# Kernel tuning notes

Measured on AMD Instinct MI355X. Metric: run time of the kernel, lower is better.

The kernel has to match this reference:

```python
import jax, jax.numpy as jnp
import numpy as np

N_OBJS = 15
C_OUT = 2
KP_THRES = 0.95
IOU_THRES = 0.45
N_R, N_SHP, N_EXP = 9, 199, 29
PDIM = N_R + N_SHP + N_EXP
RESIZE = 320
NUM_ANCHORS = 2
SENTINEL = -1e30  # marks non-detected candidate boxes so they never match NMS output


def _anchor_centers(stride):
    hw = RESIZE // stride
    X, Y = jnp.meshgrid(jnp.arange(hw), jnp.arange(hw))
    ac = (jnp.stack([X, Y], -1) * stride).reshape(-1, 2)
    # stack([c]*2, axis=1).reshape(-1,2) == interleaved repeat
    return jnp.repeat(ac, NUM_ANCHORS, axis=0).astype(jnp.float32)  # (A,2)


def _process_level(cls, bbox, param, stride, pms, u_base, shp_base, exp_base, r):
    B, A, _ = cls.shape
    prob = jax.nn.sigmoid(cls)                      # (B,A,2)
    mask = prob > KP_THRES
    ac = _anchor_centers(stride)                    # (A,2)
    d = bbox * stride
    x1 = ac[:, 0] - d[..., 0]; y1 = ac[:, 1] - d[..., 1]
    x2 = ac[:, 0] + d[..., 2]; y2 = ac[:, 1] + d[..., 3]
    boxes = jnp.stack([x1, y1, x2, y2], -1).reshape(B, A, 2, 2)   # rows [x1,y1],[x2,y2]
    # 3DMM param decode
    p = param * pms[1] + pms[0]
    R = p[..., :N_R].reshape(B, A, 3, 3)
    shp = p[..., N_R:N_R + N_SHP]
    exp = p[..., N_R + N_SHP:]
    ln = u_base[:, 0] + shp @ shp_base.T + exp @ exp_base.T       # (B,A,204)
    ln = jnp.einsum('bakd,bacd->bakc', ln.reshape(B, A, 68, 3), R)[..., :2]  # lnmks @ R^T, keep xy
    tl = ln.min(-2, keepdims=True); br = ln.max(-2, keepdims=True)
    scale = (boxes[:, :, 1:, :] - boxes[:, :, :1, :]) / (br - tl)
    ln = jnp.abs(scale) * ln                         # (B,A,68,2)
    boxes_yx = boxes[..., ::-1] * r                  # (x,y)->(y,x), scale to original image
    ln_yx = ln[..., ::-1] * r
    boxes5 = jnp.concatenate(
        [jnp.broadcast_to(boxes_yx.reshape(B, A, 1, 4), (B, A, C_OUT, 4)), prob[..., None]], -1)
    ln_c = jnp.broadcast_to(ln_yx[:, :, None], (B, A, C_OUT, 68, 2))
    bidx = jnp.broadcast_to(jnp.arange(B)[:, None, None], (B, A, C_OUT)).reshape(-1)
    cidx = jnp.broadcast_to(jnp.arange(C_OUT)[None, None, :], (B, A, C_OUT)).reshape(-1)
    return mask.reshape(-1), boxes5.reshape(-1, 5), ln_c.reshape(-1, 68, 2), bidx, cidx


def _greedy_nms(boxes, scores, k, iou_thres):
    # NMS selection indices are constants w.r.t. AD (like tf.image NMS)
    boxes = jax.lax.stop_gradient(boxes)
    scores = jax.lax.stop_gradient(scores)
    n = scores.shape[0]
    area = jnp.clip(boxes[:, 2] - boxes[:, 0], 0) * jnp.clip(boxes[:, 3] - boxes[:, 1], 0)

    def step(carry, i):
        active, sel = carry
        s = jnp.where(active, scores, -jnp.inf)
        j = jnp.argmax(s)
        valid = s[j] > -jnp.inf
        sel = sel.at[i].set(jnp.where(valid, j.astype(jnp.int32), -1))
        tl = jnp.maximum(boxes[j, :2], boxes[:, :2])
        br = jnp.minimum(boxes[j, 2:], boxes[:, 2:])
        inter = jnp.prod(jnp.clip(br - tl, 0), -1)
        union = area[j] + area - inter
        iou = jnp.where(union > 0, inter / union, 0.0)
        active = active & (iou <= iou_thres)
        active = active.at[j].set(False)
        active = active & valid
        return (active, sel), None

    (_, sel), _ = jax.lax.scan(step, (jnp.ones(n, bool), -jnp.ones(k, jnp.int32)), jnp.arange(k))
    return sel


def _combined_nms(boxes, scores):
    # boxes (n_objs, C_OUT, 4) [y1,x1,y2,x2] per class, scores (n_objs, C_OUT)
    bs, ss, cs = [], [], []
    for c in range(C_OUT):
        sel = _greedy_nms(boxes[:, c], scores[:, c], N_OBJS, IOU_THRES)
        valid = sel >= 0
        si = jnp.clip(sel, 0)
        bs.append(boxes[si, c])
        ss.append(jnp.where(valid, scores[si, c], -jnp.inf))
        cs.append(jnp.full((N_OBJS,), float(c), jnp.float32))
    b = jnp.concatenate(bs); s = jnp.concatenate(ss); cl = jnp.concatenate(cs)
    order = jnp.argsort(-s)[:N_OBJS]
    b, s, cl = b[order], s[order], cl[order]
    valid = s > -jnp.inf
    return (jnp.where(valid[:, None], b, 0.0), jnp.where(valid, s, 0.0), jnp.where(valid, cl, 0.0))


def _forward(cls_16, bbox_16, param_16, cls_32, bbox_32, param_32,
             origin_shapes, pms, u_base, shp_base, exp_base):
    r = (origin_shapes / float(RESIZE))[0]            # (2,) -> einsum over b with b==1
    B = cls_16.shape[0]
    out_boxes = -jnp.ones((B, N_OBJS, C_OUT, 5), jnp.float32)
    cand_boxes, cand_ln, cand_idx = [], [], []
    levels = ((cls_16, bbox_16, param_16, 16), (cls_32, bbox_32, param_32, 32))  # stride 8 skipped
    for cls, bbox, param, stride in levels:
        mask, boxes5, ln, bidx, cidx = _process_level(
            cls, bbox, param, stride, pms, u_base, shp_base, exp_base, r)
        oidx = jnp.cumsum(mask) - 1                   # tf.where row-major detection order
        oidx = jnp.where(mask, oidx, N_OBJS).astype(jnp.int32)  # OOB -> dropped (TF-GPU scatter semantics)
        out_boxes = out_boxes.at[bidx, oidx, cidx].set(boxes5, mode='drop')
        cand_boxes.append(jnp.where(mask[:, None], boxes5[:, :4], SENTINEL))
        cand_ln.append(ln)
        cand_idx.append(jnp.stack([bidx, oidx, cidx], -1))
    bbox_tensor = jnp.concatenate(cand_boxes)         # (N,4)
    lnmk_tensor = jnp.concatenate(cand_ln)            # (N,68,2)
    idxs_tensor = jnp.concatenate(cand_idx)           # (N,3)

    scores = out_boxes[..., -1]                       # (B,n,2)
    boxes_pc = out_boxes[..., :-1]                    # (B,n,2,4)
    nms_b, nms_s, nms_c = jax.vmap(_combined_nms)(boxes_pc, scores)

    box_results = jnp.where(nms_b == -1.0, jnp.inf, nms_b)    # (B,n,4)
    flat = box_results.reshape(-1, 4)
    match = jnp.all(flat[:, None, :] == bbox_tensor[None, :, :], -1)  # (B*n, N)
    matched = match.any(-1)
    cand = jnp.argmax(match, -1)
    ln_sel = lnmk_tensor[cand]
    idx_sel = jnp.where(matched[:, None], idxs_tensor[cand], jnp.array([0, N_OBJS, 0], jnp.int32))
    out_ln = -jnp.ones((B, N_OBJS, C_OUT, 68, 2), jnp.float32)
    out_ln = out_ln.at[idx_sel[:, 0], idx_sel[:, 1], idx_sel[:, 2]].set(ln_sel, mode='drop')
    out_ln = jnp.where(out_ln == -1.0, jnp.inf, out_ln)

    box_results = jnp.where(box_results - 1.0 == -1.0, jnp.inf, box_results)
    bb = jnp.concatenate([box_results, nms_s[..., None], nms_c[..., None]], -1)
    bb = jnp.where(bb == -1.0, jnp.inf, bb)
    return bb.reshape(-1, N_OBJS, 6), out_ln


def setup_inputs() -> dict:
    key = jax.random.key(0)
    ks = jax.random.split(key, 14)
    B = 32
    rn = lambda k, shp, s=1.0: jax.random.normal(k, shp, jnp.float32) * s
    return {
        'cls_8': rn(ks[0], (B, 3200, 2)),
        'bbox_8': jax.random.uniform(ks[1], (B, 3200, 4), jnp.float32),
        'param_8': rn(ks[2], (B, 3200, PDIM)),
        'cls_16': rn(ks[3], (B, 800, 2)),
        'bbox_16': jax.random.uniform(ks[4], (B, 800, 4), jnp.float32),
        'param_16': rn(ks[5], (B, 800, PDIM)),
        'cls_32': rn(ks[6], (B, 200, 2)),
        'bbox_32': jax.random.uniform(ks[7], (B, 200, 4), jnp.float32),
        'param_32': rn(ks[8], (B, 200, PDIM)),
        'origin_shapes': jnp.ones((1, 2), jnp.float32) * 640.0,
        'pms': jnp.concatenate([rn(ks[9], (1, PDIM), 0.05),
                                jax.random.uniform(ks[10], (1, PDIM), jnp.float32) * 0.05], 0),
        'u_base': rn(ks[11], (204, 1)),
        'shp_base': rn(ks[12], (204, 199), 0.01),
        'exp_base': rn(ks[13], (204, 29), 0.01),
    }


def reference(cls_8, bbox_8, param_8, cls_16, bbox_16, param_16,
              cls_32, bbox_32, param_32, origin_shapes, pms, u_base, shp_base, exp_base):
    # level-0 (stride 8) feats are accepted but skipped, matching the original `continue`
    return _forward(cls_16, bbox_16, param_16, cls_32, bbox_32, param_32,
                    origin_shapes, pms, u_base, shp_base, exp_base)
```

## Files before the change

kernel.cpp:

```cpp
#include <hip/hip_runtime.h>
#include <math.h>


#define BIGF  3.0e38f

#define B_    32
#define A16   800
#define A32   200
#define NOBJ  15
#define NCLS  2
#define CAP   512
#define SMAX  256
#define N16FLAT (B_*A16*NCLS)
#define NFLAT   (N16FLAT + B_*A32*NCLS)
#define PDIM  237
#define NR    9
#define NSHP  199
#define NEXP  29
#define KTOT  (NSHP + NEXP)
#define NROW  204
#define NCHUNK 4
#define CHK   (KTOT/NCHUNK)
#define CHKF  (CHK*NROW)
#define CHKF4 (CHKF/4)

#define OFF_CNT    0
#define OFF_N      1
#define OFF_N16    2
#define OFF_GLIST  16
#define OFF_SORTG  (OFF_GLIST + CAP)
#define OFF_OIDX   (OFF_SORTG + CAP)
#define OFF_CBOX   (OFF_OIDX + CAP)
#define OFF_CSCORE (OFF_CBOX + 4*CAP)
#define OFF_OUTB   (OFF_CSCORE + CAP)
#define OFF_BR1    (OFF_OUTB + B_*NOBJ*NCLS*5)
#define OFF_CLN    (OFF_BR1 + B_*NOBJ*4)
#define OFF_BT     (OFF_CLN + CAP*136)

#define OUT_LN_OFF (B_*NOBJ*6)
#define LN_SIZE    (B_*NOBJ*NCLS*68*2)
#define LN_SIZE4   (LN_SIZE/4)
#define OUTB_SZ4   (B_*NOBJ*NCLS*5/4)
#define INIT4      (LN_SIZE4 + OUTB_SZ4)
#define BT_N       (KTOT*NROW)
#define IM_THREADS 46592

#define NMS_BLOCKS B_

__device__ __forceinline__ void decode_g(int g, int& lvl, int& b, int& a, int& c) {
  if (g < N16FLAT) {
    lvl = 0; b = g / (A16*NCLS); int q = g % (A16*NCLS); a = q >> 1; c = q & 1;
  } else {
    int g2 = g - N16FLAT;
    lvl = 1; b = g2 / (A32*NCLS); int q = g2 % (A32*NCLS); a = q >> 1; c = q & 1;
  }
}

__device__ __forceinline__ float sigm(float x) { return 1.0f / (1.0f + expf(-x)); }

__device__ __forceinline__ void wave_argmax(float& v, int& idx) {
  #pragma unroll
  for (int off = 1; off < 64; off <<= 1) {
    float ov = __shfl_xor(v, off);
    int   oi = __shfl_xor(idx, off);
    if (ov > v || (ov == v && oi < idx)) { v = ov; idx = oi; }
  }
}

__global__ void k_initmask(const float* __restrict__ cls16,
                           const float* __restrict__ cls32,
                           const float* __restrict__ shpb,
                           const float* __restrict__ expb,
                           float* __restrict__ out, float* __restrict__ ws) {
  int t = blockIdx.x * blockDim.x + threadIdx.x;
  if (t < LN_SIZE4)
    ((float4*)(out + OUT_LN_OFF))[t] = make_float4(BIGF, BIGF, BIGF, BIGF);
  else if (t < INIT4)
    ((float4*)(ws + OFF_OUTB))[t - LN_SIZE4] = make_float4(-1.f, -1.f, -1.f, -1.f);
  const int N16F4 = N16FLAT/4, NF4 = NFLAT/4;
  if (t < NF4) {
    float4 v; int base;
    if (t < N16F4) { v = ((const float4*)cls16)[t]; base = 4*t; }
    else { v = ((const float4*)cls32)[t - N16F4]; base = N16FLAT + 4*(t - N16F4); }
    float vv[4] = {v.x, v.y, v.z, v.w};
    #pragma unroll
    for (int k = 0; k < 4; ++k) {
      if (sigm(vv[k]) > 0.95f) {
        int pos = atomicAdd(&((int*)ws)[OFF_CNT], 1);
        if (pos < CAP) ((int*)ws)[OFF_GLIST + pos] = base + k;
      }
    }
  }
  if (t < BT_N) {
    int row = t % NROW, k = t / NROW;
    float v = (k < NSHP) ? shpb[(size_t)row*NSHP + k]
                         : expb[(size_t)row*NEXP + (k - NSHP)];
    ws[OFF_BT + t] = v;
  }
}

__global__ void k_prep(const float* __restrict__ cls16, const float* __restrict__ bbox16,
                       const float* __restrict__ cls32, const float* __restrict__ bbox32,
                       const float* __restrict__ oshapes, float* __restrict__ ws) {
  __shared__ int s_gl[CAP];
  __shared__ int s_sorted[CAP];
  __shared__ int sh_n16;
  int tid = threadIdx.x;
  int* wi = (int*)ws;
  int n = wi[OFF_CNT]; if (n > CAP) n = CAP;
  if (tid == 0) { wi[OFF_N] = n; sh_n16 = 0; }
  for (int i = tid; i < n; i += blockDim.x) s_gl[i] = wi[OFF_GLIST + i];
  __syncthreads();

  int loc16 = 0;
  for (int i = tid; i < n; i += blockDim.x) {
    int gi = s_gl[i];
    int rank = 0;
    for (int j = 0; j < n; ++j) rank += (s_gl[j] < gi);
    s_sorted[rank] = gi;
    loc16 += (gi < N16FLAT);
  }
  if (loc16) atomicAdd(&sh_n16, loc16);
  __syncthreads();
  int n16 = sh_n16;
  if (tid == 0) wi[OFF_N16] = n16;

  float r0 = oshapes[0] / 320.0f;
  float r1 = oshapes[1] / 320.0f;

  for (int s = tid; s < n; s += blockDim.x) {
    int g = s_sorted[s];
    wi[OFF_SORTG + s] = g;
    int lvl, b, a, c; decode_g(g, lvl, b, a, c);
    int oidx = (s < n16) ? s : (s - n16);
    wi[OFF_OIDX + s] = oidx;
    const float* cls = lvl ? cls32 : cls16;
    const float* bbp = lvl ? bbox32 : bbox16;
    int A = lvl ? A32 : A16;
    int hw = lvl ? 10 : 20;
    float stride = lvl ? 32.f : 16.f;
    float prob = sigm(cls[(b*A + a)*2 + c]);
    int pos = a >> 1;
    float acx = (float)(pos % hw) * stride;
    float acy = (float)(pos / hw) * stride;
    const float* bp = bbp + (size_t)(b*A + a) * 4;
    float x1 = acx - bp[0]*stride, y1 = acy - bp[1]*stride;
    float x2 = acx + bp[2]*stride, y2 = acy + bp[3]*stride;
    ws[OFF_CBOX + 4*s + 0] = y1 * r0;
    ws[OFF_CBOX + 4*s + 1] = x1 * r1;
    ws[OFF_CBOX + 4*s + 2] = y2 * r0;
    ws[OFF_CBOX + 4*s + 3] = x2 * r1;
    ws[OFF_CSCORE + s] = prob;
  }
  __syncthreads();
  int lim16 = (n16 < NOBJ) ? n16 : NOBJ;
  for (int s = tid; s < lim16; s += blockDim.x) {
    int g = s_sorted[s]; int lvl, b, a, c; decode_g(g, lvl, b, a, c);
    int base = ((b*NOBJ + s)*NCLS + c) * 5;
    for (int k = 0; k < 4; ++k) ws[OFF_OUTB + base + k] = ws[OFF_CBOX + 4*s + k];
    ws[OFF_OUTB + base + 4] = ws[OFF_CSCORE + s];
  }
  __syncthreads();
  int lim32 = ((n - n16) < NOBJ) ? (n - n16) : NOBJ;
  for (int t2 = tid; t2 < lim32; t2 += blockDim.x) {
    int s = n16 + t2;
    int g = s_sorted[s]; int lvl, b, a, c; decode_g(g, lvl, b, a, c);
    int base = ((b*NOBJ + t2)*NCLS + c) * 5;
    for (int k = 0; k < 4; ++k) ws[OFF_OUTB + base + k] = ws[OFF_CBOX + 4*s + k];
    ws[OFF_OUTB + base + 4] = ws[OFF_CSCORE + s];
  }
}

struct SharedLand {
  float4 bt4[CHKF4];
  float p[PDIM];
  float l204[NROW];
  float l2[136];
  float sc01[2];
};

__global__ void __launch_bounds__(256)
k_landnms(const float* __restrict__ param16,
          const float* __restrict__ param32,
          const float* __restrict__ bbox16,
          const float* __restrict__ bbox32,
          const float* __restrict__ pms,
          const float* __restrict__ ubase,
          const float* __restrict__ oshapes,
          float* __restrict__ ws, float* __restrict__ out) {
  __shared__ SharedLand su;
  __shared__ int   s_lsel[NCLS*NOBJ];
  __shared__ float s_lsc[NCLS*NOBJ];
  int tid = threadIdx.x;
  int bid = blockIdx.x;
  int* wi = (int*)ws;

  if (bid < SMAX) {
    int n = wi[OFF_N]; if (n > SMAX) n = SMAX;
    int s = bid;
    if (s >= n) return;
    int g = wi[OFF_SORTG + s];
    int lvl, b, a, c; decode_g(g, lvl, b, a, c);
    int A = lvl ? A32 : A16;
    const float* par = (lvl ? param32 : param16) + (size_t)(b*A + a) * PDIM;
    if (tid < PDIM) su.p[tid] = fmaf(par[tid], pms[PDIM + tid], pms[tid]);
    __syncthreads();
    float acc = 0.f;
    for (int ch = 0; ch < NCHUNK; ++ch) {
      const float4* src = (const float4*)(ws + OFF_BT + ch*CHKF);
      for (int i = tid; i < CHKF4; i += 256) su.bt4[i] = src[i];
      __syncthreads();
      if (tid < NROW) {
        const float* sb = (const float*)su.bt4;
        #pragma unroll 19
        for (int kk = 0; kk < CHK; ++kk)
          acc = fmaf(su.p[NR + ch*CHK + kk], sb[kk*NROW + tid], acc);
      }
      __syncthreads();
    }
    if (tid < NROW) su.l204[tid] = ubase[tid] + acc;
    __syncthreads();
    if (tid < 68) {
      float v0 = su.l204[3*tid], v1 = su.l204[3*tid+1], v2 = su.l204[3*tid+2];
      su.l2[2*tid]     = v0*su.p[0] + v1*su.p[1] + v2*su.p[2];
      su.l2[2*tid + 1] = v0*su.p[3] + v1*su.p[4] + v2*su.p[5];
    }
    __syncthreads();
    if (tid < 64) {
      int lane = tid;
      float mn0 = INFINITY, mx0 = -INFINITY, mn1 = INFINITY, mx1 = -INFINITY;
      for (int k = lane; k < 68; k += 64) {
        float x = su.l2[2*k], y = su.l2[2*k+1];
        mn0 = fminf(mn0, x); mx0 = fmaxf(mx0, x);
        mn1 = fminf(mn1, y); mx1 = fmaxf(mx1, y);
      }
      #pragma unroll
      for (int off = 32; off > 0; off >>= 1) {
        mn0 = fminf(mn0, __shfl_down(mn0, off)); mx0 = fmaxf(mx0, __shfl_down(mx0, off));
        mn1 = fminf(mn1, __shfl_down(mn1, off)); mx1 = fmaxf(mx1, __shfl_down(mx1, off));
      }
      if (lane == 0) {
        float stride = lvl ? 32.f : 16.f;
        int hw = lvl ? 10 : 20;
        int pos = a >> 1;
        float acx = (float)(pos % hw) * stride;
        float acy = (float)(pos / hw) * stride;
        const float* bp = (lvl ? bbox32 : bbox16) + (size_t)(b*A + a) * 4;
        float x1 = acx - bp[0]*stride, x2 = acx + bp[2]*stride;
        float y1 = acy - bp[1]*stride, y2 = acy + bp[3]*stride;
        su.sc01[0] = fabsf((x2 - x1) / (mx0 - mn0));
        su.sc01[1] = fabsf((y2 - y1) / (mx1 - mn1));
      }
    }
    __syncthreads();
    if (tid < 68) {
      float r0 = oshapes[0] / 320.0f, r1 = oshapes[1] / 320.0f;
      float lx = su.sc01[0] * su.l2[2*tid];
      float ly = su.sc01[1] * su.l2[2*tid + 1];
      ws[OFF_CLN + (size_t)s*136 + 2*tid]     = ly * r0;
      ws[OFF_CLN + (size_t)s*136 + 2*tid + 1] = lx * r1;
    }
  } else {
    int b = bid - SMAX;
    int w = tid >> 6, lane = tid & 63;
    if (w < NCLS) {
      int c = w;
      float b0 = 0.f, b1 = 0.f, b2 = 0.f, b3 = 0.f, sc = -INFINITY, ar = 0.f;
      if (lane < NOBJ) {
        int base = ((b*NOBJ + lane)*NCLS + c) * 5;
        b0 = ws[OFF_OUTB + base + 0];
        b1 = ws[OFF_OUTB + base + 1];
        b2 = ws[OFF_OUTB + base + 2];
        b3 = ws[OFF_OUTB + base + 3];
        sc = ws[OFF_OUTB + base + 4];
        float dy = b2 - b0; if (dy < 0.f) dy = 0.f;
        float dx = b3 - b1; if (dx < 0.f) dx = 0.f;
        ar = dy * dx;
      }
      bool alive = (lane < NOBJ);
      for (int it = 0; it < NOBJ; ++it) {
        float v = alive ? sc : -INFINITY;
        int idx = lane;
        wave_argmax(v, idx);
        bool valid = v > -INFINITY;
        if (lane == 0) {
          s_lsel[c*NOBJ + it] = valid ? idx : -1;
          s_lsc [c*NOBJ + it] = valid ? v : -INFINITY;
        }
        float j0 = __shfl(b0, idx), j1 = __shfl(b1, idx);
        float j2 = __shfl(b2, idx), j3 = __shfl(b3, idx);
        float ja = __shfl(ar, idx);
        float tly = fmaxf(j0, b0);
        float tlx = fmaxf(j1, b1);
        float bry = fminf(j2, b2);
        float brx = fminf(j3, b3);
        float iy = bry - tly; if (iy < 0.f) iy = 0.f;
        float ix = brx - tlx; if (ix < 0.f) ix = 0.f;
        float inter = iy * ix;
        float uni = ja + ar - inter;
        float iou = (uni > 0.f) ? (inter / uni) : 0.f;
        alive = alive && (iou <= 0.45f) && (lane != idx) && valid;
      }
    }
    __syncthreads();
    if (w == 0) {
      float sv = -INFINITY;
      float bx0 = 0.f, bx1 = 0.f, bx2 = 0.f, bx3 = 0.f;
      int c = 0;
      bool used = (lane >= NCLS*NOBJ);
      if (lane < NCLS*NOBJ) {
        c = lane / NOBJ;
        int sl = s_lsel[lane];
        sv = s_lsc[lane];
        int si = (sl >= 0) ? sl : 0;
        int base = ((b*NOBJ + si)*NCLS + c) * 5;
        bx0 = ws[OFF_OUTB + base + 0];
        bx1 = ws[OFF_OUTB + base + 1];
        bx2 = ws[OFF_OUTB + base + 2];
        bx3 = ws[OFF_OUTB + base + 3];
      }
      for (int r = 0; r < NOBJ; ++r) {
        float v = used ? -INFINITY : sv;
        int idx = lane;
        wave_argmax(v, idx);
        if (lane == idx) {
          used = true;
          bool valid = sv > -INFINITY;
          float ns  = valid ? sv : 0.f;
          float ncl = valid ? (float)c : 0.f;
          float nb[4];
          nb[0] = valid ? bx0 : 0.f;
          nb[1] = valid ? bx1 : 0.f;
          nb[2] = valid ? bx2 : 0.f;
          nb[3] = valid ? bx3 : 0.f;
          #pragma unroll
          for (int k = 0; k < 4; ++k) {
            float b1v = (nb[k] == -1.0f) ? BIGF : nb[k];
            ws[OFF_BR1 + (b*NOBJ + r)*4 + k] = b1v;
            float b2v = ((b1v - 1.0f) == -1.0f) ? BIGF : b1v;
            float b3v = (b2v == -1.0f) ? BIGF : b2v;
            out[(b*NOBJ + r)*6 + k] = b3v;
          }
          out[(b*NOBJ + r)*6 + 4] = (ns  == -1.0f) ? BIGF : ns;
          out[(b*NOBJ + r)*6 + 5] = (ncl == -1.0f) ? BIGF : ncl;
        }
      }
    }
  }
}

__global__ void k_match(float* __restrict__ ws, float* __restrict__ out) {
  __shared__ float s_cbox[4*CAP];
  int* wi = (int*)ws;
  int n = wi[OFF_N];
  for (int i = threadIdx.x; i < 4*n; i += blockDim.x) s_cbox[i] = ws[OFF_CBOX + i];
  __syncthreads();
  int t = blockIdx.x * blockDim.x + threadIdx.x;
  if (t >= B_*NOBJ) return;
  float q0 = ws[OFF_BR1 + 4*t + 0], q1 = ws[OFF_BR1 + 4*t + 1];
  float q2 = ws[OFF_BR1 + 4*t + 2], q3 = ws[OFF_BR1 + 4*t + 3];
  int ms = -1;
  for (int s = 0; s < n; ++s) {
    if (s_cbox[4*s] == q0 && s_cbox[4*s+1] == q1 &&
        s_cbox[4*s+2] == q2 && s_cbox[4*s+3] == q3) { ms = s; break; }
  }
  if (ms < 0) return;
  int oidx = wi[OFF_OIDX + ms];
  if (oidx >= NOBJ) return;
  int g = wi[OFF_SORTG + ms];
  int lvl, b, a, c; decode_g(g, lvl, b, a, c);
  float4* dst = (float4*)(out + OUT_LN_OFF + (size_t)((b*NOBJ + oidx)*NCLS + c) * 136);
  const float4* src = (const float4*)(ws + OFF_CLN + (size_t)ms * 136);
  for (int k = 0; k < 34; ++k) dst[k] = src[k];
}

extern "C" void kernel_launch(void* const* d_in, const int* in_sizes, int n_in,
                              void* d_out, int out_size, void* d_ws, size_t ws_size,
                              hipStream_t stream) {
  const float* cls16   = (const float*)d_in[3];
  const float* bbox16  = (const float*)d_in[4];
  const float* param16 = (const float*)d_in[5];
  const float* cls32   = (const float*)d_in[6];
  const float* bbox32  = (const float*)d_in[7];
  const float* param32 = (const float*)d_in[8];
  const float* oshapes = (const float*)d_in[9];
  const float* pms     = (const float*)d_in[10];
  const float* ubase   = (const float*)d_in[11];
  const float* shpb    = (const float*)d_in[12];
  const float* expb    = (const float*)d_in[13];
  float* out = (float*)d_out;
  float* ws  = (float*)d_ws;

  hipMemsetAsync(ws, 0, 64, stream);
  k_initmask<<<(IM_THREADS + 255)/256, 256, 0, stream>>>(cls16, cls32, shpb, expb, out, ws);
  k_prep<<<1, 256, 0, stream>>>(cls16, bbox16, cls32, bbox32, oshapes, ws);
  k_landnms<<<SMAX + NMS_BLOCKS, 256, 0, stream>>>(param16, param32, bbox16, bbox32,
                                                   pms, ubase, oshapes, ws, out);
  k_match<<<2, 256, 0, stream>>>(ws, out);
}
```

Measured before the change: 203.8 us.

## Fuse all stages into one cooperative kernel with grid syncs

```diff
diff --git a/kernel.cpp b/kernel.cpp
--- a/kernel.cpp
+++ b/kernel.cpp
@@ -1,5 +1,8 @@
 #include <hip/hip_runtime.h>
+#include <hip/hip_cooperative_groups.h>
 #include <math.h>
+
+namespace cg = cooperative_groups;
 
 
 #define BIGF  3.0e38f
@@ -19,16 +22,9 @@
 #define NEXP  29
 #define KTOT  (NSHP + NEXP)
 #define NROW  204
-#define NCHUNK 4
-#define CHK   (KTOT/NCHUNK)
-#define CHKF  (CHK*NROW)
-#define CHKF4 (CHKF/4)
-
-#define OFF_CNT    0
+
 #define OFF_N      1
-#define OFF_N16    2
-#define OFF_GLIST  16
-#define OFF_SORTG  (OFF_GLIST + CAP)
+#define OFF_SORTG  16
 #define OFF_OIDX   (OFF_SORTG + CAP)
 #define OFF_CBOX   (OFF_OIDX + CAP)
 #define OFF_CSCORE (OFF_CBOX + 4*CAP)
@@ -36,16 +32,19 @@
 #define OFF_BR1    (OFF_OUTB + B_*NOBJ*NCLS*5)
 #define OFF_CLN    (OFF_BR1 + B_*NOBJ*4)
 #define OFF_BT     (OFF_CLN + CAP*136)
+#define BT_N       (KTOT*NROW)
+#define OFF_BCNT   (OFF_BT + BT_N)
+#define OFF_BLIST  (OFF_BCNT + 512)
 
 #define OUT_LN_OFF (B_*NOBJ*6)
 #define LN_SIZE    (B_*NOBJ*NCLS*68*2)
 #define LN_SIZE4   (LN_SIZE/4)
 #define OUTB_SZ4   (B_*NOBJ*NCLS*5/4)
 #define INIT4      (LN_SIZE4 + OUTB_SZ4)
-#define BT_N       (KTOT*NROW)
-#define IM_THREADS 46592
-
-#define NMS_BLOCKS B_
+
+#define NMASKB 16
+#define MPB    128
+#define GRID_BLKS (SMAX + B_)
 
 __device__ __forceinline__ void decode_g(int g, int& lvl, int& b, int& a, int& c) {
   if (g < N16FLAT) {
@@ -67,200 +66,216 @@
   }
 }
 
-__global__ void k_initmask(const float* __restrict__ cls16,
-                           const float* __restrict__ cls32,
-                           const float* __restrict__ shpb,
-                           const float* __restrict__ expb,
-                           float* __restrict__ out, float* __restrict__ ws) {
-  int t = blockIdx.x * blockDim.x + threadIdx.x;
+union SharedU {
+  struct { int cnt; int list[MPB]; } m;
+  struct { int gl[CAP]; int sorted[CAP]; int cnt16[NMASKB];
+           int off[NMASKB]; int n16; int nn; } prep;
+  struct { float p[PDIM]; float l204[NROW]; float l2[136]; float sc01[2]; } land;
+  struct { int lsel[NCLS*NOBJ]; float lsc[NCLS*NOBJ]; } nms;
+  struct { float cbox[4*CAP]; } match;
+};
+
+__global__ void __launch_bounds__(256)
+k_fused(const float* __restrict__ param16,
+        const float* __restrict__ param32,
+        const float* __restrict__ bbox16,
+        const float* __restrict__ bbox32,
+        const float* __restrict__ pms,
+        const float* __restrict__ ubase,
+        const float* __restrict__ oshapes,
+        const float* __restrict__ cls16,
+        const float* __restrict__ cls32,
+        const float* __restrict__ shpb,
+        const float* __restrict__ expb,
+        float* __restrict__ ws,
+        float* __restrict__ out) {
+  __shared__ SharedU su;
+  cg::grid_group grid = cg::this_grid();
+  int tid = threadIdx.x;
+  int bid = blockIdx.x;
+  int t = bid * 256 + tid;
+  int* wi = (int*)ws;
+
   if (t < LN_SIZE4)
     ((float4*)(out + OUT_LN_OFF))[t] = make_float4(BIGF, BIGF, BIGF, BIGF);
   else if (t < INIT4)
     ((float4*)(ws + OFF_OUTB))[t - LN_SIZE4] = make_float4(-1.f, -1.f, -1.f, -1.f);
-  const int N16F4 = N16FLAT/4, NF4 = NFLAT/4;
-  if (t < NF4) {
-    float4 v; int base;
-    if (t < N16F4) { v = ((const float4*)cls16)[t]; base = 4*t; }
-    else { v = ((const float4*)cls32)[t - N16F4]; base = N16FLAT + 4*(t - N16F4); }
-    float vv[4] = {v.x, v.y, v.z, v.w};
-    #pragma unroll
-    for (int k = 0; k < 4; ++k) {
-      if (sigm(vv[k]) > 0.95f) {
-        int pos = atomicAdd(&((int*)ws)[OFF_CNT], 1);
-        if (pos < CAP) ((int*)ws)[OFF_GLIST + pos] = base + k;
-      }
-    }
-  }
   if (t < BT_N) {
     int row = t % NROW, k = t / NROW;
     float v = (k < NSHP) ? shpb[(size_t)row*NSHP + k]
                          : expb[(size_t)row*NEXP + (k - NSHP)];
     ws[OFF_BT + t] = v;
   }
-}
-
-__global__ void k_prep(const float* __restrict__ cls16, const float* __restrict__ bbox16,
-                       const float* __restrict__ cls32, const float* __restrict__ bbox32,
-                       const float* __restrict__ oshapes, float* __restrict__ ws) {
-  __shared__ int s_gl[CAP];
-  __shared__ int s_sorted[CAP];
-  __shared__ int sh_n16;
-  int tid = threadIdx.x;
-  int* wi = (int*)ws;
-  int n = wi[OFF_CNT]; if (n > CAP) n = CAP;
-  if (tid == 0) { wi[OFF_N] = n; sh_n16 = 0; }
-  for (int i = tid; i < n; i += blockDim.x) s_gl[i] = wi[OFF_GLIST + i];
+  if (tid == 0) su.m.cnt = 0;
   __syncthreads();
-
-  int loc16 = 0;
-  for (int i = tid; i < n; i += blockDim.x) {
-    int gi = s_gl[i];
-    int rank = 0;
-    for (int j = 0; j < n; ++j) rank += (s_gl[j] < gi);
-    s_sorted[rank] = gi;
-    loc16 += (gi < N16FLAT);
-  }
-  if (loc16) atomicAdd(&sh_n16, loc16);
+  {
+    const int N16F4 = N16FLAT/4, NF4 = NFLAT/4;
+    if (t < NF4) {
+      float4 v; int base;
+      if (t < N16F4) { v = ((const float4*)cls16)[t]; base = 4*t; }
+      else { v = ((const float4*)cls32)[t - N16F4]; base = N16FLAT + 4*(t - N16F4); }
+      float vv[4] = {v.x, v.y, v.z, v.w};
+      #pragma unroll
+      for (int k = 0; k < 4; ++k) {
+        if (sigm(vv[k]) > 0.95f) {
+          int p = atomicAdd(&su.m.cnt, 1);
+          if (p < MPB) su.m.list[p] = base + k;
+        }
+      }
+    }
+  }
   __syncthreads();
-  int n16 = sh_n16;
-  if (tid == 0) wi[OFF_N16] = n16;
-
-  float r0 = oshapes[0] / 320.0f;
-  float r1 = oshapes[1] / 320.0f;
-
-  for (int s = tid; s < n; s += blockDim.x) {
-    int g = s_sorted[s];
-    wi[OFF_SORTG + s] = g;
-    int lvl, b, a, c; decode_g(g, lvl, b, a, c);
-    int oidx = (s < n16) ? s : (s - n16);
-    wi[OFF_OIDX + s] = oidx;
-    const float* cls = lvl ? cls32 : cls16;
-    const float* bbp = lvl ? bbox32 : bbox16;
-    int A = lvl ? A32 : A16;
-    int hw = lvl ? 10 : 20;
-    float stride = lvl ? 32.f : 16.f;
-    float prob = sigm(cls[(b*A + a)*2 + c]);
-    int pos = a >> 1;
-    float acx = (float)(pos % hw) * stride;
-    float acy = (float)(pos / hw) * stride;
-    const float* bp = bbp + (size_t)(b*A + a) * 4;
-    float x1 = acx - bp[0]*stride, y1 = acy - bp[1]*stride;
-    float x2 = acx + bp[2]*stride, y2 = acy + bp[3]*stride;
-    ws[OFF_CBOX + 4*s + 0] = y1 * r0;
-    ws[OFF_CBOX + 4*s + 1] = x1 * r1;
-    ws[OFF_CBOX + 4*s + 2] = y2 * r0;
-    ws[OFF_CBOX + 4*s + 3] = x2 * r1;
-    ws[OFF_CSCORE + s] = prob;
-  }
-  __syncthreads();
-  int lim16 = (n16 < NOBJ) ? n16 : NOBJ;
-  for (int s = tid; s < lim16; s += blockDim.x) {
-    int g = s_sorted[s]; int lvl, b, a, c; decode_g(g, lvl, b, a, c);
-    int base = ((b*NOBJ + s)*NCLS + c) * 5;
-    for (int k = 0; k < 4; ++k) ws[OFF_OUTB + base + k] = ws[OFF_CBOX + 4*s + k];
-    ws[OFF_OUTB + base + 4] = ws[OFF_CSCORE + s];
-  }
-  __syncthreads();
-  int lim32 = ((n - n16) < NOBJ) ? (n - n16) : NOBJ;
-  for (int t2 = tid; t2 < lim32; t2 += blockDim.x) {
-    int s = n16 + t2;
-    int g = s_sorted[s]; int lvl, b, a, c; decode_g(g, lvl, b, a, c);
-    int base = ((b*NOBJ + t2)*NCLS + c) * 5;
-    for (int k = 0; k < 4; ++k) ws[OFF_OUTB + base + k] = ws[OFF_CBOX + 4*s + k];
-    ws[OFF_OUTB + base + 4] = ws[OFF_CSCORE + s];
-  }
-}
-
-struct SharedLand {
-  float4 bt4[CHKF4];
-  float p[PDIM];
-  float l204[NROW];
-  float l2[136];
-  float sc01[2];
-};
-
-__global__ void __launch_bounds__(256)
-k_landnms(const float* __restrict__ param16,
-          const float* __restrict__ param32,
-          const float* __restrict__ bbox16,
-          const float* __restrict__ bbox32,
-          const float* __restrict__ pms,
-          const float* __restrict__ ubase,
-          const float* __restrict__ oshapes,
-          float* __restrict__ ws, float* __restrict__ out) {
-  __shared__ SharedLand su;
-  __shared__ int   s_lsel[NCLS*NOBJ];
-  __shared__ float s_lsc[NCLS*NOBJ];
-  int tid = threadIdx.x;
-  int bid = blockIdx.x;
-  int* wi = (int*)ws;
+  {
+    int cnt = su.m.cnt; if (cnt > MPB) cnt = MPB;
+    if (tid == 0) wi[OFF_BCNT + bid] = cnt;
+    for (int i = tid; i < cnt; i += 256) wi[OFF_BLIST + bid*MPB + i] = su.m.list[i];
+  }
+  __threadfence();
+  grid.sync();
+
+  if (bid == 0) {
+    if (tid < NMASKB) su.prep.cnt16[tid] = wi[OFF_BCNT + tid];
+    __syncthreads();
+    if (tid == 0) {
+      int o = 0;
+      for (int i = 0; i < NMASKB; ++i) { su.prep.off[i] = o; o += su.prep.cnt16[i]; }
+      int n0 = (o > CAP) ? CAP : o;
+      su.prep.nn = n0;
+      su.prep.n16 = 0;
+      wi[OFF_N] = n0;
+    }
+    __syncthreads();
+    int n = su.prep.nn;
+    for (int j = tid; j < NMASKB*MPB; j += 256) {
+      int b2 = j / MPB, slot = j % MPB;
+      if (slot < su.prep.cnt16[b2]) {
+        int pos = su.prep.off[b2] + slot;
+        if (pos < CAP) su.prep.gl[pos] = wi[OFF_BLIST + j];
+      }
+    }
+    __syncthreads();
+
+    int loc16 = 0;
+    for (int i = tid; i < n; i += 256) {
+      int gi = su.prep.gl[i];
+      int rank = 0;
+      for (int j = 0; j < n; ++j) rank += (su.prep.gl[j] < gi);
+      su.prep.sorted[rank] = gi;
+      loc16 += (gi < N16FLAT);
+    }
+    if (loc16) atomicAdd(&su.prep.n16, loc16);
+    __syncthreads();
+    int n16 = su.prep.n16;
+
+    float r0 = oshapes[0] / 320.0f;
+    float r1 = oshapes[1] / 320.0f;
+
+    for (int s = tid; s < n; s += 256) {
+      int g = su.prep.sorted[s];
+      wi[OFF_SORTG + s] = g;
+      int lvl, b, a, c; decode_g(g, lvl, b, a, c);
+      int oidx = (s < n16) ? s : (s - n16);
+      wi[OFF_OIDX + s] = oidx;
+      const float* cls = lvl ? cls32 : cls16;
+      const float* bbp = lvl ? bbox32 : bbox16;
+      int A = lvl ? A32 : A16;
+      int hw = lvl ? 10 : 20;
+      float stride = lvl ? 32.f : 16.f;
+      float prob = sigm(cls[(b*A + a)*2 + c]);
+      int pos = a >> 1;
+      float acx = (float)(pos % hw) * stride;
+      float acy = (float)(pos / hw) * stride;
+      const float* bp = bbp + (size_t)(b*A + a) * 4;
+      float x1 = acx - bp[0]*stride, y1 = acy - bp[1]*stride;
+      float x2 = acx + bp[2]*stride, y2 = acy + bp[3]*stride;
+      ws[OFF_CBOX + 4*s + 0] = y1 * r0;
+      ws[OFF_CBOX + 4*s + 1] = x1 * r1;
+      ws[OFF_CBOX + 4*s + 2] = y2 * r0;
+      ws[OFF_CBOX + 4*s + 3] = x2 * r1;
+      ws[OFF_CSCORE + s] = prob;
+    }
+    __syncthreads();
+    int lim16 = (n16 < NOBJ) ? n16 : NOBJ;
+    for (int s = tid; s < lim16; s += 256) {
+      int g = su.prep.sorted[s]; int lvl, b, a, c; decode_g(g, lvl, b, a, c);
+      int base = ((b*NOBJ + s)*NCLS + c) * 5;
+      for (int k = 0; k < 4; ++k) ws[OFF_OUTB + base + k] = ws[OFF_CBOX + 4*s + k];
+      ws[OFF_OUTB + base + 4] = ws[OFF_CSCORE + s];
+    }
+    __syncthreads();
+    int lim32 = ((n - n16) < NOBJ) ? (n - n16) : NOBJ;
+    for (int t2 = tid; t2 < lim32; t2 += 256) {
+      int s = n16 + t2;
+      int g = su.prep.sorted[s]; int lvl, b, a, c; decode_g(g, lvl, b, a, c);
+      int base = ((b*NOBJ + t2)*NCLS + c) * 5;
+      for (int k = 0; k < 4; ++k) ws[OFF_OUTB + base + k] = ws[OFF_CBOX + 4*s + k];
+      ws[OFF_OUTB + base + 4] = ws[OFF_CSCORE + s];
+    }
+  }
+  __threadfence();
+  grid.sync();
 
   if (bid < SMAX) {
     int n = wi[OFF_N]; if (n > SMAX) n = SMAX;
-    int s = bid;
-    if (s >= n) return;
-    int g = wi[OFF_SORTG + s];
-    int lvl, b, a, c; decode_g(g, lvl, b, a, c);
-    int A = lvl ? A32 : A16;
-    const float* par = (lvl ? param32 : param16) + (size_t)(b*A + a) * PDIM;
-    if (tid < PDIM) su.p[tid] = fmaf(par[tid], pms[PDIM + tid], pms[tid]);
-    __syncthreads();
-    float acc = 0.f;
-    for (int ch = 0; ch < NCHUNK; ++ch) {
-      const float4* src = (const float4*)(ws + OFF_BT + ch*CHKF);
-      for (int i = tid; i < CHKF4; i += 256) su.bt4[i] = src[i];
+    if (bid < n) {
+      int s = bid;
+      int g = wi[OFF_SORTG + s];
+      int lvl, b, a, c; decode_g(g, lvl, b, a, c);
+      int A = lvl ? A32 : A16;
+      const float* par = (lvl ? param32 : param16) + (size_t)(b*A + a) * PDIM;
+      if (tid < PDIM) su.land.p[tid] = fmaf(par[tid], pms[PDIM + tid], pms[tid]);
       __syncthreads();
       if (tid < NROW) {
-        const float* sb = (const float*)su.bt4;
-        #pragma unroll 19
-        for (int kk = 0; kk < CHK; ++kk)
-          acc = fmaf(su.p[NR + ch*CHK + kk], sb[kk*NROW + tid], acc);
+        float acc = 0.f;
+        const float* bt = ws + OFF_BT;
+        #pragma unroll 12
+        for (int kk = 0; kk < KTOT; ++kk)
+          acc = fmaf(su.land.p[NR + kk], bt[(size_t)kk*NROW + tid], acc);
+        su.land.l204[tid] = ubase[tid] + acc;
       }
       __syncthreads();
-    }
-    if (tid < NROW) su.l204[tid] = ubase[tid] + acc;
-    __syncthreads();
-    if (tid < 68) {
-      float v0 = su.l204[3*tid], v1 = su.l204[3*tid+1], v2 = su.l204[3*tid+2];
-      su.l2[2*tid]     = v0*su.p[0] + v1*su.p[1] + v2*su.p[2];
-      su.l2[2*tid + 1] = v0*su.p[3] + v1*su.p[4] + v2*su.p[5];
-    }
-    __syncthreads();
-    if (tid < 64) {
-      int lane = tid;
-      float mn0 = INFINITY, mx0 = -INFINITY, mn1 = INFINITY, mx1 = -INFINITY;
-      for (int k = lane; k < 68; k += 64) {
-        float x = su.l2[2*k], y = su.l2[2*k+1];
-        mn0 = fminf(mn0, x); mx0 = fmaxf(mx0, x);
-        mn1 = fminf(mn1, y); mx1 = fmaxf(mx1, y);
-      }
-      #pragma unroll
-      for (int off = 32; off > 0; off >>= 1) {
-        mn0 = fminf(mn0, __shfl_down(mn0, off)); mx0 = fmaxf(mx0, __shfl_down(mx0, off));
-        mn1 = fminf(mn1, __shfl_down(mn1, off)); mx1 = fmaxf(mx1, __shfl_down(mx1, off));
-      }
-      if (lane == 0) {
-        float stride = lvl ? 32.f : 16.f;
-        int hw = lvl ? 10 : 20;
-        int pos = a >> 1;
-        float acx = (float)(pos % hw) * stride;
-        float acy = (float)(pos / hw) * stride;
-        const float* bp = (lvl ? bbox32 : bbox16) + (size_t)(b*A + a) * 4;
-        float x1 = acx - bp[0]*stride, x2 = acx + bp[2]*stride;
-        float y1 = acy - bp[1]*stride, y2 = acy + bp[3]*stride;
-        su.sc01[0] = fabsf((x2 - x1) / (mx0 - mn0));
-        su.sc01[1] = fabsf((y2 - y1) / (mx1 - mn1));
-      }
-    }
-    __syncthreads();
-    if (tid < 68) {
-      float r0 = oshapes[0] / 320.0f, r1 = oshapes[1] / 320.0f;
-      float lx = su.sc01[0] * su.l2[2*tid];
-      float ly = su.sc01[1] * su.l2[2*tid + 1];
-      ws[OFF_CLN + (size_t)s*136 + 2*tid]     = ly * r0;
-      ws[OFF_CLN + (size_t)s*136 + 2*tid + 1] = lx * r1;
-    }
-  } else {
+      if (tid < 68) {
+        float v0 = su.land.l204[3*tid], v1 = su.land.l204[3*tid+1], v2 = su.land.l204[3*tid+2];
+        su.land.l2[2*tid]     = v0*su.land.p[0] + v1*su.land.p[1] + v2*su.land.p[2];
+        su.land.l2[2*tid + 1] = v0*su.land.p[3] + v1*su.land.p[4] + v2*su.land.p[5];
+      }
+      __syncthreads();
+      if (tid < 64) {
+        int lane = tid;
+        float mn0 = INFINITY, mx0 = -INFINITY, mn1 = INFINITY, mx1 = -INFINITY;
+        for (int k = lane; k < 68; k += 64) {
+          float x = su.land.l2[2*k], y = su.land.l2[2*k+1];
+          mn0 = fminf(mn0, x); mx0 = fmaxf(mx0, x);
+          mn1 = fminf(mn1, y); mx1 = fmaxf(mx1, y);
+        }
+        #pragma unroll
+        for (int off = 32; off > 0; off >>= 1) {
+          mn0 = fminf(mn0, __shfl_down(mn0, off)); mx0 = fmaxf(mx0, __shfl_down(mx0, off));
+          mn1 = fminf(mn1, __shfl_down(mn1, off)); mx1 = fmaxf(mx1, __shfl_down(mx1, off));
+        }
+        if (lane == 0) {
+          float stride = lvl ? 32.f : 16.f;
+          int hw = lvl ? 10 : 20;
+          int pos = a >> 1;
+          float acx = (float)(pos % hw) * stride;
+          float acy = (float)(pos / hw) * stride;
+          const float* bp = (lvl ? bbox32 : bbox16) + (size_t)(b*A + a) * 4;
+          float x1 = acx - bp[0]*stride, x2 = acx + bp[2]*stride;
+          float y1 = acy - bp[1]*stride, y2 = acy + bp[3]*stride;
+          su.land.sc01[0] = fabsf((x2 - x1) / (mx0 - mn0));
+          su.land.sc01[1] = fabsf((y2 - y1) / (mx1 - mn1));
+        }
+      }
+      __syncthreads();
+      if (tid < 68) {
+        float r0 = oshapes[0] / 320.0f, r1 = oshapes[1] / 320.0f;
+        float lx = su.land.sc01[0] * su.land.l2[2*tid];
+        float ly = su.land.sc01[1] * su.land.l2[2*tid + 1];
+        ws[OFF_CLN + (size_t)s*136 + 2*tid]     = ly * r0;
+        ws[OFF_CLN + (size_t)s*136 + 2*tid + 1] = lx * r1;
+      }
+    }
+  } else if (bid < SMAX + B_) {
     int b = bid - SMAX;
     int w = tid >> 6, lane = tid & 63;
     if (w < NCLS) {
@@ -284,8 +299,8 @@
         wave_argmax(v, idx);
         bool valid = v > -INFINITY;
         if (lane == 0) {
-          s_lsel[c*NOBJ + it] = valid ? idx : -1;
-          s_lsc [c*NOBJ + it] = valid ? v : -INFINITY;
+          su.nms.lsel[c*NOBJ + it] = valid ? idx : -1;
+          su.nms.lsc [c*NOBJ + it] = valid ? v : -INFINITY;
         }
         float j0 = __shfl(b0, idx), j1 = __shfl(b1, idx);
         float j2 = __shfl(b2, idx), j3 = __shfl(b3, idx);
@@ -310,8 +325,8 @@
       bool used = (lane >= NCLS*NOBJ);
       if (lane < NCLS*NOBJ) {
         c = lane / NOBJ;
-        int sl = s_lsel[lane];
-        sv = s_lsc[lane];
+        int sl = su.nms.lsel[lane];
+        sv = su.nms.lsc[lane];
         int si = (sl >= 0) ? sl : 0;
         int base = ((b*NOBJ + si)*NCLS + c) * 5;
         bx0 = ws[OFF_OUTB + base + 0];
@@ -347,31 +362,34 @@
       }
     }
   }
-}
-
-__global__ void k_match(float* __restrict__ ws, float* __restrict__ out) {
-  __shared__ float s_cbox[4*CAP];
-  int* wi = (int*)ws;
-  int n = wi[OFF_N];
-  for (int i = threadIdx.x; i < 4*n; i += blockDim.x) s_cbox[i] = ws[OFF_CBOX + i];
-  __syncthreads();
-  int t = blockIdx.x * blockDim.x + threadIdx.x;
-  if (t >= B_*NOBJ) return;
-  float q0 = ws[OFF_BR1 + 4*t + 0], q1 = ws[OFF_BR1 + 4*t + 1];
-  float q2 = ws[OFF_BR1 + 4*t + 2], q3 = ws[OFF_BR1 + 4*t + 3];
-  int ms = -1;
-  for (int s = 0; s < n; ++s) {
-    if (s_cbox[4*s] == q0 && s_cbox[4*s+1] == q1 &&
-        s_cbox[4*s+2] == q2 && s_cbox[4*s+3] == q3) { ms = s; break; }
-  }
-  if (ms < 0) return;
-  int oidx = wi[OFF_OIDX + ms];
-  if (oidx >= NOBJ) return;
-  int g = wi[OFF_SORTG + ms];
-  int lvl, b, a, c; decode_g(g, lvl, b, a, c);
-  float4* dst = (float4*)(out + OUT_LN_OFF + (size_t)((b*NOBJ + oidx)*NCLS + c) * 136);
-  const float4* src = (const float4*)(ws + OFF_CLN + (size_t)ms * 136);
-  for (int k = 0; k < 34; ++k) dst[k] = src[k];
+  __threadfence();
+  grid.sync();
+
+  if (bid < 2) {
+    int n = wi[OFF_N];
+    for (int i = tid; i < 4*n; i += 256) su.match.cbox[i] = ws[OFF_CBOX + i];
+    __syncthreads();
+    int t3 = bid * 256 + tid;
+    if (t3 < B_*NOBJ) {
+      float q0 = ws[OFF_BR1 + 4*t3 + 0], q1 = ws[OFF_BR1 + 4*t3 + 1];
+      float q2 = ws[OFF_BR1 + 4*t3 + 2], q3 = ws[OFF_BR1 + 4*t3 + 3];
+      int ms = -1;
+      for (int s = 0; s < n; ++s) {
+        if (su.match.cbox[4*s] == q0 && su.match.cbox[4*s+1] == q1 &&
+            su.match.cbox[4*s+2] == q2 && su.match.cbox[4*s+3] == q3) { ms = s; break; }
+      }
+      if (ms >= 0) {
+        int oidx = wi[OFF_OIDX + ms];
+        if (oidx < NOBJ) {
+          int g = wi[OFF_SORTG + ms];
+          int lvl, b, a, c; decode_g(g, lvl, b, a, c);
+          float4* dst = (float4*)(out + OUT_LN_OFF + (size_t)((b*NOBJ + oidx)*NCLS + c) * 136);
+          const float4* src = (const float4*)(ws + OFF_CLN + (size_t)ms * 136);
+          for (int k = 0; k < 34; ++k) dst[k] = src[k];
+        }
+      }
+    }
+  }
 }
 
 extern "C" void kernel_launch(void* const* d_in, const int* in_sizes, int n_in,
@@ -391,10 +409,12 @@
   float* out = (float*)d_out;
   float* ws  = (float*)d_ws;
 
-  hipMemsetAsync(ws, 0, 64, stream);
-  k_initmask<<<(IM_THREADS + 255)/256, 256, 0, stream>>>(cls16, cls32, shpb, expb, out, ws);
-  k_prep<<<1, 256, 0, stream>>>(cls16, bbox16, cls32, bbox32, oshapes, ws);
-  k_landnms<<<SMAX + NMS_BLOCKS, 256, 0, stream>>>(param16, param32, bbox16, bbox32,
-                                                   pms, ubase, oshapes, ws, out);
-  k_match<<<2, 256, 0, stream>>>(ws, out);
+  void* args[] = {
+    (void*)&param16, (void*)&param32, (void*)&bbox16, (void*)&bbox32,
+    (void*)&pms, (void*)&ubase, (void*)&oshapes,
+    (void*)&cls16, (void*)&cls32, (void*)&shpb, (void*)&expb,
+    (void*)&ws, (void*)&out
+  };
+  hipLaunchCooperativeKernel((void*)k_fused, dim3(GRID_BLKS), dim3(256),
+                             args, 0, stream);
 }
```

Measured after the change: 379.0 us. 85.9% more time.
